# Performance work log

Hardware: AMD Instinct MI355X
Metric: run time of the kernel (lower is better)

The kernel has to match this reference:

```python
import jax, jax.numpy as jnp
import numpy as np

HIDDEN = 1024
N_HEAD = 16
HEAD_DIM = HIDDEN // N_HEAD  # 64
BATCH = 1
SEQ = 4096
THETA = 10000.0


def _rope_cos_sin(seq_len, head_dim, dtype=jnp.float32):
    # freqs[t, j] = t / theta^(2j/dim), j in [0, dim/2)
    inv_freq = 1.0 / (THETA ** (jnp.arange(0, head_dim, 2, dtype=dtype) / head_dim))
    t = jnp.arange(seq_len, dtype=dtype)
    freqs = jnp.outer(t, inv_freq)           # [S, D/2]
    return jnp.cos(freqs), jnp.sin(freqs)


def _apply_rope(x, cos, sin):
    # x: [B, S, H, D]; pairs (x[...,2j], x[...,2j+1]) rotated by angle freqs[t, j]
    x2 = x.reshape(*x.shape[:-1], -1, 2)       # [B, S, H, D/2, 2]
    x_re, x_im = x2[..., 0], x2[..., 1]
    c = cos[None, :, None, :]                   # [1, S, 1, D/2]
    s = sin[None, :, None, :]
    out_re = x_re * c - x_im * s
    out_im = x_re * s + x_im * c
    out = jnp.stack([out_re, out_im], axis=-1)  # [B, S, H, D/2, 2]
    return out.reshape(x.shape)


def setup_inputs() -> dict:
    key = jax.random.key(0)
    kx, kq, kk, kv = jax.random.split(key, 4)
    scale = 1.0 / np.sqrt(HIDDEN)
    return {
        "x": jax.random.normal(kx, (BATCH, SEQ, HIDDEN), dtype=jnp.float32),
        "wq": jax.random.normal(kq, (HIDDEN, HIDDEN), dtype=jnp.float32) * scale,
        "wk": jax.random.normal(kk, (HIDDEN, HIDDEN), dtype=jnp.float32) * scale,
        "wv": jax.random.normal(kv, (HIDDEN, HIDDEN), dtype=jnp.float32) * scale,
    }


def reference(x, wq, wk, wv):
    B, S, _ = x.shape
    # torch nn.Linear(no bias): y = x @ W.T
    xq = (x @ wq.T).reshape(B, S, N_HEAD, HEAD_DIM).astype(jnp.float32)
    xk = (x @ wk.T).reshape(B, S, N_HEAD, HEAD_DIM).astype(jnp.float32)
    xv = (x @ wv.T).reshape(B, S, N_HEAD, HEAD_DIM).astype(jnp.float32)

    cos, sin = _rope_cos_sin(S, HEAD_DIM)
    q = _apply_rope(xq, cos, sin)
    k = _apply_rope(xk, cos, sin)

    # [B, H, S, S] scores, no causal mask (matches source)
    scores = jnp.einsum("bqhd,bkhd->bhqk", q, k) / jnp.sqrt(
        jnp.asarray(HEAD_DIM, dtype=q.dtype))
    attn = jax.nn.softmax(scores, axis=-1)
    out = jnp.einsum("bhqk,bkhd->bqhd", attn, xv)  # [B, S, H, D]
    return out.reshape(B, S, N_HEAD * HEAD_DIM)
```

## Files before the change

### kernel.cpp

```cpp
#include <hip/hip_runtime.h>
#include <stdint.h>


#define SEQLEN 4096
#define NHEAD 16
#define HDIM 64

typedef __bf16 bf16x8 __attribute__((ext_vector_type(8)));
typedef float f32x4 __attribute__((ext_vector_type(4)));
typedef float f32x16 __attribute__((ext_vector_type(16)));

__device__ __forceinline__ unsigned short f2bf(float f) {
  union { float f; unsigned int u; } v; v.f = f;
  unsigned int r = v.u + 0x7FFFu + ((v.u >> 16) & 1u);
  return (unsigned short)(r >> 16);
}
__device__ __forceinline__ unsigned int pkc(float lo, float hi) {
  union { __bf16 b[2]; unsigned int u; } z;
  z.b[0] = (__bf16)lo; z.b[1] = (__bf16)hi;
  return z.u;
}
__device__ __forceinline__ bf16x8 as_bf(uint4 v) { return __builtin_bit_cast(bf16x8, v); }
__device__ __forceinline__ f32x4 mfma16(bf16x8 a, bf16x8 b, f32x4 c) {
  return __builtin_amdgcn_mfma_f32_16x16x32_bf16(a, b, c, 0, 0, 0);
}
__device__ __forceinline__ f32x16 mfma32(bf16x8 a, bf16x8 b, f32x16 c) {
  return __builtin_amdgcn_mfma_f32_32x32x16_bf16(a, b, c, 0, 0, 0);
}
__device__ __forceinline__ uint2 mku2(unsigned x, unsigned y) {
  uint2 r; r.x = x; r.y = y; return r;
}

__global__ __launch_bounds__(256) void k_convert(
    const float* __restrict__ x, const float* __restrict__ wq,
    const float* __restrict__ wk, const float* __restrict__ wv,
    unsigned short* __restrict__ xbf, unsigned short* __restrict__ wbf) {
  int i = blockIdx.x * 256 + threadIdx.x;
  const int NX = SEQLEN * 1024 / 4;
  const int NW = 1024 * 1024 / 4;
  float4 v;
  unsigned short* dst;
  int di;
  if (i < NX) {
    v = ((const float4*)x)[i]; dst = xbf; di = i;
  } else {
    int j = i - NX;
    const float4* src = (const float4*)((j < NW) ? wq : (j < 2 * NW) ? wk : wv);
    v = src[j & (NW - 1)];
    dst = wbf; di = j;
  }
  ushort4 o; o.x = f2bf(v.x); o.y = f2bf(v.y); o.z = f2bf(v.z); o.w = f2bf(v.w);
  ((ushort4*)dst)[di] = o;
}

__global__ __launch_bounds__(256) void k_table(float* __restrict__ ct, float* __restrict__ st) {
  int i = blockIdx.x * 256 + threadIdx.x;
  int s = i >> 5, j = i & 31;
  double inv = exp(-(double)j * 0.28782313662425572);
  double a = (double)s * inv;
  ct[i] = (float)cos(a);
  st[i] = (float)sin(a);
}

__global__ __launch_bounds__(256) void k_gemm(
    const unsigned short* __restrict__ xbf, const unsigned short* __restrict__ wbf,
    const float* __restrict__ ct, const float* __restrict__ st,
    unsigned short* __restrict__ qbf, unsigned short* __restrict__ kbf,
    unsigned short* __restrict__ vT) {
  __shared__ __align__(16) unsigned short As[2][128 * 40];
  __shared__ __align__(16) unsigned short Bs[2][128 * 40];
  const int t = threadIdx.x;
  const int bn = blockIdx.x, bm = blockIdx.y;
  const int lane = t & 63, wave = t >> 6;
  const int r = lane & 15, g = lane >> 4;
  const int wm = wave >> 1, wn = wave & 1;

  const int c0 = t, c1 = t + 256;
  const int ar0 = c0 >> 2, ao0 = (c0 & 3) * 16;
  const int ar1 = c1 >> 2, ao1 = (c1 & 3) * 16;

  const char* pA0 = (const char*)xbf + (size_t)(bm * 128 + ar0) * 2048 + ao0;
  const char* pA1 = (const char*)xbf + (size_t)(bm * 128 + ar1) * 2048 + ao1;
  const char* pB0 = (const char*)wbf + (size_t)(bn * 128 + ar0) * 2048 + ao0;
  const char* pB1 = (const char*)wbf + (size_t)(bn * 128 + ar1) * 2048 + ao1;

  uint4 ra0, ra1, rb0, rb1;
#define LD_TILE                                   \
  ra0 = *(const uint4*)pA0; ra1 = *(const uint4*)pA1; \
  rb0 = *(const uint4*)pB0; rb1 = *(const uint4*)pB1; \
  pA0 += 64; pA1 += 64; pB0 += 64; pB1 += 64;

  LD_TILE
  f32x4 zero4 = {0.f, 0.f, 0.f, 0.f};
  f32x4 acc[4][4];
#pragma unroll
  for (int m = 0; m < 4; ++m)
#pragma unroll
    for (int n = 0; n < 4; ++n) acc[m][n] = zero4;

  for (int kk = 0; kk < 32; ++kk) {
    unsigned short* Ac = As[kk & 1];
    unsigned short* Bc = Bs[kk & 1];
    *(uint4*)((char*)Ac + ar0 * 80 + ao0) = ra0;
    *(uint4*)((char*)Ac + ar1 * 80 + ao1) = ra1;
    *(uint4*)((char*)Bc + ar0 * 80 + ao0) = rb0;
    *(uint4*)((char*)Bc + ar1 * 80 + ao1) = rb1;
    __syncthreads();
    if (kk < 31) { LD_TILE }
    bf16x8 af[4], bfr[4];
#pragma unroll
    for (int m = 0; m < 4; ++m)
      af[m] = as_bf(*(const uint4*)((const char*)Ac + (wm * 64 + m * 16 + r) * 80 + g * 16));
#pragma unroll
    for (int n = 0; n < 4; ++n)
      bfr[n] = as_bf(*(const uint4*)((const char*)Bc + (wn * 64 + n * 16 + r) * 80 + g * 16));
#pragma unroll
    for (int m = 0; m < 4; ++m)
#pragma unroll
      for (int n = 0; n < 4; ++n)
        acc[m][n] = mfma16(af[m], bfr[n], acc[m][n]);
  }

  const int matid = bn >> 3;
#pragma unroll
  for (int m = 0; m < 4; ++m) {
    const int row0 = bm * 128 + wm * 64 + m * 16 + 4 * g;
#pragma unroll
    for (int n = 0; n < 4; ++n) {
      const int col = bn * 128 + wn * 64 + n * 16 + r;
      const int d = col & 63;
      const int hh = (col >> 6) & 15;
      if (matid < 2) {
        const int jdx = (col >> 1) & 31;
        const float sgn = (col & 1) ? 1.0f : -1.0f;
        unsigned short* dst = (matid == 0) ? qbf : kbf;
        const float qs = (matid == 0) ? 0.18033688011112042f : 1.0f;
#pragma unroll
        for (int j = 0; j < 4; ++j) {
          float v = acc[m][n][j];
          float p = __shfl_xor(v, 1);
          int srow = row0 + j;
          float cv = ct[srow * 32 + jdx];
          float sv = st[srow * 32 + jdx];
          float o = (v * cv + p * sv * sgn) * qs;
          dst[(size_t)srow * 1024 + (hh * 64 + d)] = f2bf(o);
        }
      } else {
        ushort4 o;
        o.x = f2bf(acc[m][n][0]); o.y = f2bf(acc[m][n][1]);
        o.z = f2bf(acc[m][n][2]); o.w = f2bf(acc[m][n][3]);
        *(ushort4*)&vT[((size_t)(hh * 64 + d)) * SEQLEN + row0] = o;
      }
    }
  }
}

__global__ __launch_bounds__(512) void k_attn(
    const unsigned short* __restrict__ qbf, const unsigned short* __restrict__ kbf,
    const unsigned short* __restrict__ vT, float* __restrict__ out) {
  __shared__ __align__(16) char smem[33280];
  const int t = threadIdx.x;
  const int b = blockIdx.x;
  const int work = (b & 7) * 64 + (b >> 3);
  const int h = work >> 5;
  const int qb = work & 31;
  const int lane = t & 63, wave = t >> 6;
  const int qw = wave & 3, hf = wave >> 2;
  const int li = lane & 31, hi = lane >> 5;
  const int q0 = qb * 128 + qw * 32;
  const int HB = hf * 16384;

  bf16x8 qf[4];
#pragma unroll
  for (int c = 0; c < 4; ++c)
    qf[c] = as_bf(*(const uint4*)((const char*)qbf +
              (size_t)(q0 + li) * 2048 + h * 128 + c * 32 + hi * 16));

  f32x16 z16 = {0.f};
  f32x16 acc[2];
  acc[0] = z16; acc[1] = z16;
  float l4[4] = {0.f, 0.f, 0.f, 0.f};

  const int mmK = (li & 15) ^ (hi << 1);
  int kra[4];
#pragma unroll
  for (int c = 0; c < 4; ++c)
    kra[c] = HB + li * 128 + ((((4 * c) ^ mmK)) << 3);
  const int mmV = (li & 15) ^ hi;
  int vra[2][2];
#pragma unroll
  for (int dt = 0; dt < 2; ++dt)
#pragma unroll
    for (int kc = 0; kc < 2; ++kc)
      vra[dt][kc] = HB + 8192 + li * 128 + ((((dt * 8 + 4 * kc) ^ mmV)) << 3);

  const int tt = t & 255;
  const int kr = tt >> 3, c8 = tt & 7;
  const int vd = tt >> 2, c4 = tt & 3;
  const int wka = HB + kr * 128 + ((((2 * c8) ^ (kr & 15))) << 3);
  const int wva = HB + 8192 + (vd & 31) * 128 +
                  (((((vd >> 5) * 8 + 2 * c4) ^ (vd & 15))) << 3);

  const char* pK = (const char*)kbf + h * 128 +
                   (size_t)(hf * 2048 + kr) * 2048 + c8 * 16;
  const char* pV = (const char*)vT + (size_t)h * HDIM * SEQLEN * 2 +
                   (size_t)vd * 8192 + hf * 4096 + c4 * 16;

  uint4 rk, rv;
#define LD_KV32                                       \
  rk = *(const uint4*)pK; rv = *(const uint4*)pV;     \
  pK += 32 * 2048; pV += 64;

  LD_KV32

#pragma unroll 2
  for (int j = 0; j < 64; ++j) {
    const int JB = (j & 1) * 4096;
    *(uint2*)(smem + (wka + JB)) = mku2(rk.x, rk.y);
    *(uint2*)(smem + ((wka ^ 8) + JB)) = mku2(rk.z, rk.w);
    *(uint2*)(smem + (wva + JB)) = mku2(rv.x, rv.y);
    *(uint2*)(smem + ((wva ^ 8) + JB)) = mku2(rv.z, rv.w);
    __syncthreads();
    if (j < 63) { LD_KV32 }

    f32x16 sT = z16;
    __builtin_amdgcn_s_setprio(1);
#pragma unroll
    for (int c = 0; c < 4; ++c) {
      uint2 a0 = *(const uint2*)(smem + (kra[c] + JB));
      uint2 a1 = *(const uint2*)(smem + ((kra[c] ^ 8) + JB));
      uint4 ku; ku.x = a0.x; ku.y = a0.y; ku.z = a1.x; ku.w = a1.y;
      sT = mfma32(as_bf(ku), qf[c], sT);
    }
    __builtin_amdgcn_s_setprio(0);

    bf16x8 vf[2][2];
#pragma unroll
    for (int dt = 0; dt < 2; ++dt)
#pragma unroll
      for (int kc = 0; kc < 2; ++kc) {
        uint2 lo = *(const uint2*)(smem + (vra[dt][kc] + JB));
        uint2 hi2 = *(const uint2*)(smem + ((vra[dt][kc] ^ 16) + JB));
        uint4 vv; vv.x = lo.x; vv.y = lo.y; vv.z = hi2.x; vv.w = hi2.y;
        vf[dt][kc] = as_bf(vv);
      }

#pragma unroll
    for (int i = 0; i < 16; ++i) sT[i] = __builtin_amdgcn_exp2f(sT[i]);

#pragma unroll
    for (int i = 0; i < 4; ++i)
      l4[i] += (sT[i] + sT[i + 4]) + (sT[i + 8] + sT[i + 12]);

    bf16x8 pfr[2];
#pragma unroll
    for (int kc = 0; kc < 2; ++kc) {
      const int bix = kc * 8;
      uint4 bw;
      bw.x = pkc(sT[bix + 0], sT[bix + 1]);
      bw.y = pkc(sT[bix + 2], sT[bix + 3]);
      bw.z = pkc(sT[bix + 4], sT[bix + 5]);
      bw.w = pkc(sT[bix + 6], sT[bix + 7]);
      pfr[kc] = as_bf(bw);
    }
    __builtin_amdgcn_s_setprio(1);
#pragma unroll
    for (int kc = 0; kc < 2; ++kc) {
      acc[0] = mfma32(vf[0][kc], pfr[kc], acc[0]);
      acc[1] = mfma32(vf[1][kc], pfr[kc], acc[1]);
    }
    __builtin_amdgcn_s_setprio(0);
  }

  float lrun = (l4[0] + l4[1]) + (l4[2] + l4[3]);
  float lhalf = lrun + __shfl_xor(lrun, 32);

  __syncthreads();
  float* shm = (float*)smem;
  if (hf == 1) {
    float* ab = shm + qw * 2048;
#pragma unroll
    for (int dt = 0; dt < 2; ++dt)
#pragma unroll
      for (int i = 0; i < 16; ++i) {
        int d = (i & 3) + 8 * (i >> 2) + 4 * hi + 32 * dt;
        ab[d * 32 + li] = acc[dt][i];
      }
    if (hi == 0) shm[8192 + qw * 32 + li] = lhalf;
  }
  __syncthreads();
  if (hf == 0) {
    float* ab = shm + qw * 2048;
    float l1 = shm[8192 + qw * 32 + li];
    float linv = 1.0f / (lhalf + l1);
#pragma unroll
    for (int dt = 0; dt < 2; ++dt)
#pragma unroll
      for (int i = 0; i < 16; ++i) {
        int d = (i & 3) + 8 * (i >> 2) + 4 * hi + 32 * dt;
        acc[dt][i] = (acc[dt][i] + ab[d * 32 + li]) * linv;
      }
    __asm__ volatile("" ::: "memory");

    float* eb = shm + qw * 2048;
#pragma unroll
    for (int dt = 0; dt < 2; ++dt) {
#pragma unroll
      for (int i = 0; i < 16; ++i)
        eb[li * 33 + ((i & 3) + 8 * (i >> 2) + 4 * hi)] = acc[dt][i];
      __asm__ volatile("" ::: "memory");
#pragma unroll
      for (int it = 0; it < 16; ++it) {
        int q = it * 2 + hi;
        float v = eb[q * 33 + li];
        out[(size_t)(q0 + q) * 1024 + h * 64 + dt * 32 + li] = v;
      }
      __asm__ volatile("" ::: "memory");
    }
  }
}

extern "C" void kernel_launch(void* const* d_in, const int* in_sizes, int n_in,
                              void* d_out, int out_size, void* d_ws, size_t ws_size,
                              hipStream_t stream) {
  const float* x  = (const float*)d_in[0];
  const float* wq = (const float*)d_in[1];
  const float* wk = (const float*)d_in[2];
  const float* wv = (const float*)d_in[3];
  float* out = (float*)d_out;
  char* ws = (char*)d_ws;

  unsigned short* qbf = (unsigned short*)(ws);
  unsigned short* kbf = (unsigned short*)(ws + ((size_t)8 << 20));
  unsigned short* vT  = (unsigned short*)(ws + ((size_t)16 << 20));
  unsigned short* xbf = (unsigned short*)(ws + ((size_t)24 << 20));
  unsigned short* wbf = (unsigned short*)(ws + ((size_t)32 << 20));
  float* ct = (float*)(ws + ((size_t)38 << 20));
  float* st = (float*)(ws + ((size_t)38 << 20) + ((size_t)512 << 10));

  k_convert<<<dim3(7168), dim3(256), 0, stream>>>(x, wq, wk, wv, xbf, wbf);
  k_table<<<dim3(512), dim3(256), 0, stream>>>(ct, st);
  k_gemm<<<dim3(24, 32), dim3(256), 0, stream>>>(xbf, wbf, ct, st, qbf, kbf, vT);
  k_attn<<<dim3(512), dim3(512), 0, stream>>>(qbf, kbf, vT, out);
}
```

Before: 149.4 us.

## Store K and V in MFMA fragment order and load directly from global

The projection GEMM now writes K and V in a pre-swizzled layout that matches the MFMA operand fragments of the attention kernel. The attention kernel drops the LDS staging, the block barriers and the register prefetch, and loads K/V fragments straight from global memory with 16-byte loads each iteration. This removes LDS traffic and per-tile __syncthreads. In exchange, global loads are now exposed without explicit double buffering, each wave re-reads K/V from L2 rather than sharing it through LDS, and the GEMM epilogue does scattered 2-byte K stores.

```diff
diff --git a/kernel.cpp b/kernel.cpp
--- a/kernel.cpp
+++ b/kernel.cpp
@@ -26,9 +26,6 @@
 }
 __device__ __forceinline__ f32x16 mfma32(bf16x8 a, bf16x8 b, f32x16 c) {
   return __builtin_amdgcn_mfma_f32_32x32x16_bf16(a, b, c, 0, 0, 0);
-}
-__device__ __forceinline__ uint2 mku2(unsigned x, unsigned y) {
-  uint2 r; r.x = x; r.y = y; return r;
 }
 
 __global__ __launch_bounds__(256) void k_convert(
@@ -65,8 +62,8 @@
 __global__ __launch_bounds__(256) void k_gemm(
     const unsigned short* __restrict__ xbf, const unsigned short* __restrict__ wbf,
     const float* __restrict__ ct, const float* __restrict__ st,
-    unsigned short* __restrict__ qbf, unsigned short* __restrict__ kbf,
-    unsigned short* __restrict__ vT) {
+    unsigned short* __restrict__ qbf, unsigned short* __restrict__ KF,
+    unsigned short* __restrict__ VF) {
   __shared__ __align__(16) unsigned short As[2][128 * 40];
   __shared__ __align__(16) unsigned short Bs[2][128 * 40];
   const int t = threadIdx.x;
@@ -133,7 +130,6 @@
       if (matid < 2) {
         const int jdx = (col >> 1) & 31;
         const float sgn = (col & 1) ? 1.0f : -1.0f;
-        unsigned short* dst = (matid == 0) ? qbf : kbf;
         const float qs = (matid == 0) ? 0.18033688011112042f : 1.0f;
 #pragma unroll
         for (int j = 0; j < 4; ++j) {
@@ -143,21 +139,33 @@
           float cv = ct[srow * 32 + jdx];
           float sv = st[srow * 32 + jdx];
           float o = (v * cv + p * sv * sgn) * qs;
-          dst[(size_t)srow * 1024 + (hh * 64 + d)] = f2bf(o);
+          if (matid == 0) {
+            qbf[(size_t)srow * 1024 + (hh * 64 + d)] = f2bf(o);
+          } else {
+            size_t kfi = (size_t)hh * 262144 + (size_t)(srow >> 5) * 2048 +
+                         (size_t)((d >> 4) & 3) * 512 +
+                         (size_t)((((d >> 3) & 1) * 32) + (srow & 31)) * 8 + (d & 7);
+            KF[kfi] = f2bf(o);
+          }
         }
       } else {
         ushort4 o;
         o.x = f2bf(acc[m][n][0]); o.y = f2bf(acc[m][n][1]);
         o.z = f2bf(acc[m][n][2]); o.w = f2bf(acc[m][n][3]);
-        *(ushort4*)&vT[((size_t)(hh * 64 + d)) * SEQLEN + row0] = o;
+        const int kt = row0 >> 5, q4 = (row0 >> 2) & 7;
+        const int kc = q4 >> 2, bb = (q4 >> 1) & 1, h2 = q4 & 1;
+        const int dt = d >> 5, l2 = d & 31;
+        size_t off = (size_t)hh * 524288 + (size_t)kt * 4096 + (size_t)dt * 2048 +
+                     (size_t)kc * 1024 + (size_t)(h2 * 32 + l2) * 16 + bb * 8;
+        *(ushort4*)((char*)VF + off) = o;
       }
     }
   }
 }
 
 __global__ __launch_bounds__(512) void k_attn(
-    const unsigned short* __restrict__ qbf, const unsigned short* __restrict__ kbf,
-    const unsigned short* __restrict__ vT, float* __restrict__ out) {
+    const unsigned short* __restrict__ qbf, const unsigned short* __restrict__ KF,
+    const unsigned short* __restrict__ VF, float* __restrict__ out) {
   __shared__ __align__(16) char smem[33280];
   const int t = threadIdx.x;
   const int b = blockIdx.x;
@@ -168,7 +176,6 @@
   const int qw = wave & 3, hf = wave >> 2;
   const int li = lane & 31, hi = lane >> 5;
   const int q0 = qb * 128 + qw * 32;
-  const int HB = hf * 16384;
 
   bf16x8 qf[4];
 #pragma unroll
@@ -181,69 +188,27 @@
   acc[0] = z16; acc[1] = z16;
   float l4[4] = {0.f, 0.f, 0.f, 0.f};
 
-  const int mmK = (li & 15) ^ (hi << 1);
-  int kra[4];
-#pragma unroll
-  for (int c = 0; c < 4; ++c)
-    kra[c] = HB + li * 128 + ((((4 * c) ^ mmK)) << 3);
-  const int mmV = (li & 15) ^ hi;
-  int vra[2][2];
-#pragma unroll
-  for (int dt = 0; dt < 2; ++dt)
-#pragma unroll
-    for (int kc = 0; kc < 2; ++kc)
-      vra[dt][kc] = HB + 8192 + li * 128 + ((((dt * 8 + 4 * kc) ^ mmV)) << 3);
-
-  const int tt = t & 255;
-  const int kr = tt >> 3, c8 = tt & 7;
-  const int vd = tt >> 2, c4 = tt & 3;
-  const int wka = HB + kr * 128 + ((((2 * c8) ^ (kr & 15))) << 3);
-  const int wva = HB + 8192 + (vd & 31) * 128 +
-                  (((((vd >> 5) * 8 + 2 * c4) ^ (vd & 15))) << 3);
-
-  const char* pK = (const char*)kbf + h * 128 +
-                   (size_t)(hf * 2048 + kr) * 2048 + c8 * 16;
-  const char* pV = (const char*)vT + (size_t)h * HDIM * SEQLEN * 2 +
-                   (size_t)vd * 8192 + hf * 4096 + c4 * 16;
-
-  uint4 rk, rv;
-#define LD_KV32                                       \
-  rk = *(const uint4*)pK; rv = *(const uint4*)pV;     \
-  pK += 32 * 2048; pV += 64;
-
-  LD_KV32
-
-#pragma unroll 2
+  const char* pK = (const char*)KF + (size_t)h * 524288 + (size_t)hf * 262144 + lane * 16;
+  const char* pV = (const char*)VF + (size_t)h * 524288 + (size_t)hf * 262144 + lane * 16;
+
   for (int j = 0; j < 64; ++j) {
-    const int JB = (j & 1) * 4096;
-    *(uint2*)(smem + (wka + JB)) = mku2(rk.x, rk.y);
-    *(uint2*)(smem + ((wka ^ 8) + JB)) = mku2(rk.z, rk.w);
-    *(uint2*)(smem + (wva + JB)) = mku2(rv.x, rv.y);
-    *(uint2*)(smem + ((wva ^ 8) + JB)) = mku2(rv.z, rv.w);
-    __syncthreads();
-    if (j < 63) { LD_KV32 }
+    bf16x8 kf[4];
+#pragma unroll
+    for (int c = 0; c < 4; ++c)
+      kf[c] = as_bf(*(const uint4*)(pK + c * 1024));
+    bf16x8 vf2[2][2];
+#pragma unroll
+    for (int dt = 0; dt < 2; ++dt)
+#pragma unroll
+      for (int kc = 0; kc < 2; ++kc)
+        vf2[dt][kc] = as_bf(*(const uint4*)(pV + dt * 2048 + kc * 1024));
 
     f32x16 sT = z16;
     __builtin_amdgcn_s_setprio(1);
 #pragma unroll
-    for (int c = 0; c < 4; ++c) {
-      uint2 a0 = *(const uint2*)(smem + (kra[c] + JB));
-      uint2 a1 = *(const uint2*)(smem + ((kra[c] ^ 8) + JB));
-      uint4 ku; ku.x = a0.x; ku.y = a0.y; ku.z = a1.x; ku.w = a1.y;
-      sT = mfma32(as_bf(ku), qf[c], sT);
-    }
+    for (int c = 0; c < 4; ++c)
+      sT = mfma32(kf[c], qf[c], sT);
     __builtin_amdgcn_s_setprio(0);
-
-    bf16x8 vf[2][2];
-#pragma unroll
-    for (int dt = 0; dt < 2; ++dt)
-#pragma unroll
-      for (int kc = 0; kc < 2; ++kc) {
-        uint2 lo = *(const uint2*)(smem + (vra[dt][kc] + JB));
-        uint2 hi2 = *(const uint2*)(smem + ((vra[dt][kc] ^ 16) + JB));
-        uint4 vv; vv.x = lo.x; vv.y = lo.y; vv.z = hi2.x; vv.w = hi2.y;
-        vf[dt][kc] = as_bf(vv);
-      }
 
 #pragma unroll
     for (int i = 0; i < 16; ++i) sT[i] = __builtin_amdgcn_exp2f(sT[i]);
@@ -266,10 +231,11 @@
     __builtin_amdgcn_s_setprio(1);
 #pragma unroll
     for (int kc = 0; kc < 2; ++kc) {
-      acc[0] = mfma32(vf[0][kc], pfr[kc], acc[0]);
-      acc[1] = mfma32(vf[1][kc], pfr[kc], acc[1]);
+      acc[0] = mfma32(vf2[0][kc], pfr[kc], acc[0]);
+      acc[1] = mfma32(vf2[1][kc], pfr[kc], acc[1]);
     }
     __builtin_amdgcn_s_setprio(0);
+    pK += 4096; pV += 4096;
   }
 
   float lrun = (l4[0] + l4[1]) + (l4[2] + l4[3]);
@@ -331,8 +297,8 @@
   char* ws = (char*)d_ws;
 
   unsigned short* qbf = (unsigned short*)(ws);
-  unsigned short* kbf = (unsigned short*)(ws + ((size_t)8 << 20));
-  unsigned short* vT  = (unsigned short*)(ws + ((size_t)16 << 20));
+  unsigned short* KF  = (unsigned short*)(ws + ((size_t)8 << 20));
+  unsigned short* VF  = (unsigned short*)(ws + ((size_t)16 << 20));
   unsigned short* xbf = (unsigned short*)(ws + ((size_t)24 << 20));
   unsigned short* wbf = (unsigned short*)(ws + ((size_t)32 << 20));
   float* ct = (float*)(ws + ((size_t)38 << 20));
@@ -340,6 +306,6 @@
 
   k_convert<<<dim3(7168), dim3(256), 0, stream>>>(x, wq, wk, wv, xbf, wbf);
   k_table<<<dim3(512), dim3(256), 0, stream>>>(ct, st);
-  k_gemm<<<dim3(24, 32), dim3(256), 0, stream>>>(xbf, wbf, ct, st, qbf, kbf, vT);
-  k_attn<<<dim3(512), dim3(512), 0, stream>>>(qbf, kbf, vT, out);
-}
+  k_gemm<<<dim3(24, 32), dim3(256), 0, stream>>>(xbf, wbf, ct, st, qbf, KF, VF);
+  k_attn<<<dim3(512), dim3(512), 0, stream>>>(qbf, KF, VF, out);
+}
```

Result: slower. 159.3 us (+6.7%).

## Use direct global-to-LDS loads in projection GEMM and merge prep kernels

Applied to the files above, without the earlier changes.

Replaces the register-staged global loads and LDS stores in the QKV GEMM with global_load_lds 16-byte transfers that write straight into unpadded LDS tiles, issued one tile ahead as double buffering. It also merges the bf16 conversion and RoPE table kernels into one launch and packs cos/sin into a float2 table so each epilogue lookup is a single load. The aim is to cut VGPR staging, LDS store instructions and one kernel launch. The cost is that the unpadded 64-byte LDS row stride may cause bank conflicts on fragment reads, and there is no explicit vmcnt wait before the barrier, which relies on the compiler to order the async loads correctly.

```diff
diff --git a/kernel.cpp b/kernel.cpp
--- a/kernel.cpp
+++ b/kernel.cpp
@@ -30,67 +30,70 @@
 __device__ __forceinline__ uint2 mku2(unsigned x, unsigned y) {
   uint2 r; r.x = x; r.y = y; return r;
 }
-
-__global__ __launch_bounds__(256) void k_convert(
+__device__ __forceinline__ void gll16(const void* g, void* l) {
+  __builtin_amdgcn_global_load_lds(
+      (const __attribute__((address_space(1))) void*)g,
+      (__attribute__((address_space(3))) void*)l, 16, 0, 0);
+}
+
+__global__ __launch_bounds__(256) void k_prep(
     const float* __restrict__ x, const float* __restrict__ wq,
     const float* __restrict__ wk, const float* __restrict__ wv,
-    unsigned short* __restrict__ xbf, unsigned short* __restrict__ wbf) {
-  int i = blockIdx.x * 256 + threadIdx.x;
+    unsigned short* __restrict__ xbf, unsigned short* __restrict__ wbf,
+    float2* __restrict__ ctst) {
   const int NX = SEQLEN * 1024 / 4;
   const int NW = 1024 * 1024 / 4;
-  float4 v;
-  unsigned short* dst;
-  int di;
-  if (i < NX) {
-    v = ((const float4*)x)[i]; dst = xbf; di = i;
+  if (blockIdx.x < 7168) {
+    int i = blockIdx.x * 256 + threadIdx.x;
+    float4 v;
+    unsigned short* dst;
+    int di;
+    if (i < NX) {
+      v = ((const float4*)x)[i]; dst = xbf; di = i;
+    } else {
+      int j = i - NX;
+      const float4* src = (const float4*)((j < NW) ? wq : (j < 2 * NW) ? wk : wv);
+      v = src[j & (NW - 1)];
+      dst = wbf; di = j;
+    }
+    ushort4 o; o.x = f2bf(v.x); o.y = f2bf(v.y); o.z = f2bf(v.z); o.w = f2bf(v.w);
+    ((ushort4*)dst)[di] = o;
   } else {
-    int j = i - NX;
-    const float4* src = (const float4*)((j < NW) ? wq : (j < 2 * NW) ? wk : wv);
-    v = src[j & (NW - 1)];
-    dst = wbf; di = j;
-  }
-  ushort4 o; o.x = f2bf(v.x); o.y = f2bf(v.y); o.z = f2bf(v.z); o.w = f2bf(v.w);
-  ((ushort4*)dst)[di] = o;
-}
-
-__global__ __launch_bounds__(256) void k_table(float* __restrict__ ct, float* __restrict__ st) {
-  int i = blockIdx.x * 256 + threadIdx.x;
-  int s = i >> 5, j = i & 31;
-  double inv = exp(-(double)j * 0.28782313662425572);
-  double a = (double)s * inv;
-  ct[i] = (float)cos(a);
-  st[i] = (float)sin(a);
+    int i = (blockIdx.x - 7168) * 256 + threadIdx.x;
+    int s = i >> 5, j = i & 31;
+    double inv = exp(-(double)j * 0.28782313662425572);
+    double a = (double)s * inv;
+    float2 cs; cs.x = (float)cos(a); cs.y = (float)sin(a);
+    ctst[i] = cs;
+  }
 }
 
 __global__ __launch_bounds__(256) void k_gemm(
     const unsigned short* __restrict__ xbf, const unsigned short* __restrict__ wbf,
-    const float* __restrict__ ct, const float* __restrict__ st,
+    const float2* __restrict__ ctst,
     unsigned short* __restrict__ qbf, unsigned short* __restrict__ kbf,
     unsigned short* __restrict__ vT) {
-  __shared__ __align__(16) unsigned short As[2][128 * 40];
-  __shared__ __align__(16) unsigned short Bs[2][128 * 40];
+  __shared__ __align__(16) unsigned short As[2][128 * 32];
+  __shared__ __align__(16) unsigned short Bs[2][128 * 32];
   const int t = threadIdx.x;
   const int bn = blockIdx.x, bm = blockIdx.y;
   const int lane = t & 63, wave = t >> 6;
   const int r = lane & 15, g = lane >> 4;
   const int wm = wave >> 1, wn = wave & 1;
 
-  const int c0 = t, c1 = t + 256;
-  const int ar0 = c0 >> 2, ao0 = (c0 & 3) * 16;
-  const int ar1 = c1 >> 2, ao1 = (c1 & 3) * 16;
-
-  const char* pA0 = (const char*)xbf + (size_t)(bm * 128 + ar0) * 2048 + ao0;
-  const char* pA1 = (const char*)xbf + (size_t)(bm * 128 + ar1) * 2048 + ao1;
-  const char* pB0 = (const char*)wbf + (size_t)(bn * 128 + ar0) * 2048 + ao0;
-  const char* pB1 = (const char*)wbf + (size_t)(bn * 128 + ar1) * 2048 + ao1;
-
-  uint4 ra0, ra1, rb0, rb1;
-#define LD_TILE                                   \
-  ra0 = *(const uint4*)pA0; ra1 = *(const uint4*)pA1; \
-  rb0 = *(const uint4*)pB0; rb1 = *(const uint4*)pB1; \
-  pA0 += 64; pA1 += 64; pB0 += 64; pB1 += 64;
-
-  LD_TILE
+  const int c0 = 2 * wave, c1 = 2 * wave + 1;
+  const int srowA = lane >> 2, sb = (lane & 3) * 16;
+  const char* gA0 = (const char*)xbf + (size_t)(bm * 128 + 16 * c0 + srowA) * 2048 + sb;
+  const char* gA1 = (const char*)xbf + (size_t)(bm * 128 + 16 * c1 + srowA) * 2048 + sb;
+  const char* gB0 = (const char*)wbf + (size_t)(bn * 128 + 16 * c0 + srowA) * 2048 + sb;
+  const char* gB1 = (const char*)wbf + (size_t)(bn * 128 + 16 * c1 + srowA) * 2048 + sb;
+
+  gll16(gA0, (char*)As[0] + c0 * 1024);
+  gll16(gA1, (char*)As[0] + c1 * 1024);
+  gll16(gB0, (char*)Bs[0] + c0 * 1024);
+  gll16(gB1, (char*)Bs[0] + c1 * 1024);
+  gA0 += 64; gA1 += 64; gB0 += 64; gB1 += 64;
+
   f32x4 zero4 = {0.f, 0.f, 0.f, 0.f};
   f32x4 acc[4][4];
 #pragma unroll
@@ -99,21 +102,25 @@
     for (int n = 0; n < 4; ++n) acc[m][n] = zero4;
 
   for (int kk = 0; kk < 32; ++kk) {
-    unsigned short* Ac = As[kk & 1];
-    unsigned short* Bc = Bs[kk & 1];
-    *(uint4*)((char*)Ac + ar0 * 80 + ao0) = ra0;
-    *(uint4*)((char*)Ac + ar1 * 80 + ao1) = ra1;
-    *(uint4*)((char*)Bc + ar0 * 80 + ao0) = rb0;
-    *(uint4*)((char*)Bc + ar1 * 80 + ao1) = rb1;
     __syncthreads();
-    if (kk < 31) { LD_TILE }
+    if (kk < 31) {
+      char* Ad = (char*)As[(kk + 1) & 1];
+      char* Bd = (char*)Bs[(kk + 1) & 1];
+      gll16(gA0, Ad + c0 * 1024);
+      gll16(gA1, Ad + c1 * 1024);
+      gll16(gB0, Bd + c0 * 1024);
+      gll16(gB1, Bd + c1 * 1024);
+      gA0 += 64; gA1 += 64; gB0 += 64; gB1 += 64;
+    }
+    const char* Ac = (const char*)As[kk & 1];
+    const char* Bc = (const char*)Bs[kk & 1];
     bf16x8 af[4], bfr[4];
 #pragma unroll
     for (int m = 0; m < 4; ++m)
-      af[m] = as_bf(*(const uint4*)((const char*)Ac + (wm * 64 + m * 16 + r) * 80 + g * 16));
+      af[m] = as_bf(*(const uint4*)(Ac + (wm * 64 + m * 16 + r) * 64 + g * 16));
 #pragma unroll
     for (int n = 0; n < 4; ++n)
-      bfr[n] = as_bf(*(const uint4*)((const char*)Bc + (wn * 64 + n * 16 + r) * 80 + g * 16));
+      bfr[n] = as_bf(*(const uint4*)(Bc + (wn * 64 + n * 16 + r) * 64 + g * 16));
 #pragma unroll
     for (int m = 0; m < 4; ++m)
 #pragma unroll
@@ -140,9 +147,8 @@
           float v = acc[m][n][j];
           float p = __shfl_xor(v, 1);
           int srow = row0 + j;
-          float cv = ct[srow * 32 + jdx];
-          float sv = st[srow * 32 + jdx];
-          float o = (v * cv + p * sv * sgn) * qs;
+          float2 cs = ctst[srow * 32 + jdx];
+          float o = (v * cs.x + p * cs.y * sgn) * qs;
           dst[(size_t)srow * 1024 + (hh * 64 + d)] = f2bf(o);
         }
       } else {
@@ -335,11 +341,9 @@
   unsigned short* vT  = (unsigned short*)(ws + ((size_t)16 << 20));
   unsigned short* xbf = (unsigned short*)(ws + ((size_t)24 << 20));
   unsigned short* wbf = (unsigned short*)(ws + ((size_t)32 << 20));
-  float* ct = (float*)(ws + ((size_t)38 << 20));
-  float* st = (float*)(ws + ((size_t)38 << 20) + ((size_t)512 << 10));
-
-  k_convert<<<dim3(7168), dim3(256), 0, stream>>>(x, wq, wk, wv, xbf, wbf);
-  k_table<<<dim3(512), dim3(256), 0, stream>>>(ct, st);
-  k_gemm<<<dim3(24, 32), dim3(256), 0, stream>>>(xbf, wbf, ct, st, qbf, kbf, vT);
+  float2* ctst = (float2*)(ws + ((size_t)38 << 20));
+
+  k_prep<<<dim3(7680), dim3(256), 0, stream>>>(x, wq, wk, wv, xbf, wbf, ctst);
+  k_gemm<<<dim3(24, 32), dim3(256), 0, stream>>>(xbf, wbf, ctst, qbf, kbf, vT);
   k_attn<<<dim3(512), dim3(512), 0, stream>>>(qbf, kbf, vT, out);
 }
```

Result: no change. 149.1 us (-0.2%).
